# Performance work log

Hardware: AMD Instinct MI355X
Metric: run time of the kernel (lower is better)

The kernel has to match this reference:

```python
import jax, jax.numpy as jnp
import numpy as np

N, IN_DIM, OUT_DIM, HEADS = 8192, 256, 64, 2

def setup_inputs() -> dict:
    key = jax.random.key(0)
    k1, k2, k3, k4, k5 = jax.random.split(key, 5)
    x = jax.random.normal(k1, (N, IN_DIM), dtype=jnp.float32)
    adj = jax.random.randint(k2, (N, N), 0, 2, dtype=jnp.int32)
    # nn.Linear(in_dim, out_dim*heads, bias=False): weight [out_dim*heads, in_dim]
    W = jax.random.normal(k3, (OUT_DIM * HEADS, IN_DIM), dtype=jnp.float32) / np.sqrt(IN_DIM)
    attn_l = jax.random.normal(k4, (HEADS, OUT_DIM), dtype=jnp.float32)
    attn_r = jax.random.normal(k5, (HEADS, OUT_DIM), dtype=jnp.float32)
    return {"x": x, "adj": adj, "W": W, "attn_l": attn_l, "attn_r": attn_r}

def reference(x, adj, W, attn_l, attn_r):
    n = x.shape[0]
    h = (x @ W.T).reshape(n, HEADS, OUT_DIM)          # [N, H, D]
    el = jnp.einsum('nhd,hd->nh', h, attn_l)           # [N, H]
    er = jnp.einsum('nhd,hd->nh', h, attn_r)           # [N, H]
    e = el[:, None, :] + er[None, :, :]                # [N, N, H]
    e = jnp.where(adj[:, :, None] == 0, -jnp.inf, e)
    a = jax.nn.softmax(e, axis=1)                      # softmax over source nodes j
    out = jnp.einsum('ijh,jhd->ihd', a, h)             # [N, H, D]
    return out.reshape(n, HEADS * OUT_DIM)
```

## Files before the change

kernel.cpp:

```cpp
#include <hip/hip_runtime.h>
#include <cstdint>
#include <cstddef>

#define N_NODES 8192
#define IN_DIM  256
#define OUT_DIM 64
#define HEADS   2
#define FEAT    128
#define NTILES  9
#define ACC_STRIDE 132
#define KSPLIT  8

typedef __bf16 bf16x8 __attribute__((ext_vector_type(8)));
typedef float  f32x4  __attribute__((ext_vector_type(4)));
typedef int    i32x4  __attribute__((ext_vector_type(4)));
typedef unsigned uu32x4 __attribute__((ext_vector_type(4)));

static __device__ __forceinline__ unsigned short f2bf(float f) {
  unsigned u = __float_as_uint(f);
  u += 0x7FFFu + ((u >> 16) & 1u);
  return (unsigned short)(u >> 16);
}

__global__ __launch_bounds__(256) void k_prep(const float* __restrict__ x,
                                              const float* __restrict__ W,
                                              const float* __restrict__ attn_r,
                                              uint4* __restrict__ frag) {
  const int kb = blockIdx.x;
  const int tid = threadIdx.x;
  const int tx = tid & 15, ty = tid >> 4;
  const int j0 = kb * 32;

  __shared__ float xs[32][68];
  __shared__ float wl[128][68];
  __shared__ unsigned short pk[32][146];

  float acc[2][8] = {};

  for (int kc = 0; kc < IN_DIM; kc += 64) {
    __syncthreads();
#pragma unroll
    for (int p = 0; p < 2; p++) {
      const int slot = p*256 + tid;
      const int r = slot >> 4, k4 = slot & 15;
      *(float4*)&xs[r][k4*4] = *(const float4*)(x + (size_t)(j0 + r)*IN_DIM + kc + k4*4);
    }
#pragma unroll
    for (int p = 0; p < 8; p++) {
      const int slot = p*256 + tid;
      const int r = slot >> 4, k4 = slot & 15;
      *(float4*)&wl[r][k4*4] = *(const float4*)(W + (size_t)r*IN_DIM + kc + k4*4);
    }
    __syncthreads();
#pragma unroll
    for (int k4 = 0; k4 < 16; k4++) {
      float4 xr[2], wr[8];
#pragma unroll
      for (int i = 0; i < 2; i++) xr[i] = *(const float4*)&xs[ty + i*16][k4*4];
#pragma unroll
      for (int jj = 0; jj < 8; jj++) wr[jj] = *(const float4*)&wl[tx + jj*16][k4*4];
#pragma unroll
      for (int i = 0; i < 2; i++)
#pragma unroll
        for (int jj = 0; jj < 8; jj++)
          acc[i][jj] += xr[i].x*wr[jj].x + xr[i].y*wr[jj].y +
                        xr[i].z*wr[jj].z + xr[i].w*wr[jj].w;
    }
  }

  float ar[8];
#pragma unroll
  for (int jj = 0; jj < 8; jj++)
    ar[jj] = attn_r[((jj >> 2)) * OUT_DIM + ((tx + jj*16) & 63)];
  float e0[2] = {}, e1[2] = {};
#pragma unroll
  for (int i = 0; i < 2; i++) {
#pragma unroll
    for (int jj = 0; jj < 4; jj++) e0[i] += acc[i][jj] * ar[jj];
#pragma unroll
    for (int jj = 4; jj < 8; jj++) e1[i] += acc[i][jj] * ar[jj];
  }
#pragma unroll
  for (int m = 1; m <= 8; m <<= 1) {
#pragma unroll
    for (int i = 0; i < 2; i++) {
      e0[i] += __shfl_xor(e0[i], m);
      e1[i] += __shfl_xor(e1[i], m);
    }
  }
  float w0[2], w1[2];
#pragma unroll
  for (int i = 0; i < 2; i++) { w0[i] = __expf(e0[i]); w1[i] = __expf(e1[i]); }

#pragma unroll
  for (int i = 0; i < 2; i++) {
    const int row = ty + i*16;
#pragma unroll
    for (int jj = 0; jj < 8; jj++)
      pk[row][tx + jj*16] = f2bf((jj < 4 ? w0[i] : w1[i]) * acc[i][jj]);
    pk[row][128 + tx] = (tx == 0) ? f2bf(w0[i]) : (tx == 1) ? f2bf(w1[i]) : 0;
  }
  __syncthreads();

#pragma unroll
  for (int t = 0; t < 3; t++) {
    const int wid = t*256 + tid;
    if (wid < 576) {
      const int l = wid & 63, n = wid >> 6;
      const int col = n*16 + (l & 15), jb = (l >> 4) * 8;
      uint4 o;
      o.x = (unsigned)pk[jb+0][col] | ((unsigned)pk[jb+1][col] << 16);
      o.y = (unsigned)pk[jb+2][col] | ((unsigned)pk[jb+3][col] << 16);
      o.z = (unsigned)pk[jb+4][col] | ((unsigned)pk[jb+5][col] << 16);
      o.w = (unsigned)pk[jb+6][col] | ((unsigned)pk[jb+7][col] << 16);
      frag[((size_t)kb*NTILES + n)*64 + l] = o;
    }
  }
}

__global__ __launch_bounds__(256, 2) void k_main(const int* __restrict__ adj,
                                                 const uint4* __restrict__ fragB,
                                                 float* __restrict__ accum) {
  const int mb = blockIdx.x >> 3;
  const int ks = blockIdx.x & 7;
  const int tid = threadIdx.x;
  const int wave = tid >> 6, lane = tid & 63;
  const int m16 = lane & 15, quad = lane >> 4;

  __shared__ int tile[2][4096];

  const int lr = lane >> 3;
  const int lc = ((lane & 7) ^ lr) << 2;
  const int kb0 = ks * 1024;
  const int* gbase = adj + (size_t)(mb*128)*N_NODES + kb0 + (size_t)lr*N_NODES + lc;

  auto stage = [&](int buf, int kk) {
#pragma unroll
    for (int i = 0; i < 4; ++i) {
      const int c = wave*4 + i;
      const int* g = gbase + (size_t)(c*8)*N_NODES + kk*32;
      __builtin_amdgcn_global_load_lds(
        (const __attribute__((address_space(1))) void*)g,
        (__attribute__((address_space(3))) void*)&tile[buf][c*256],
        16, 0, 0);
    }
  };

  const int r0 = wave*32 + m16;
  const int swz = (r0 & 7) << 4;
  const int a0off = r0*128 + ((quad*32) ^ swz);
  const uu32x4* bb = (const uu32x4*)fragB + lane;

  f32x4 acc0[NTILES], acc1[NTILES];
#pragma unroll
  for (int n = 0; n < NTILES; n++) {
    acc0[n] = (f32x4){0.f, 0.f, 0.f, 0.f};
    acc1[n] = (f32x4){0.f, 0.f, 0.f, 0.f};
  }

  auto conv8 = [&](i32x4 lo, i32x4 hi) -> bf16x8 {
    unsigned u0 = (lo[0] ? 0x3F80u : 0u) | (lo[1] ? 0x3F800000u : 0u);
    unsigned u1 = (lo[2] ? 0x3F80u : 0u) | (lo[3] ? 0x3F800000u : 0u);
    unsigned u2 = (hi[0] ? 0x3F80u : 0u) | (hi[1] ? 0x3F800000u : 0u);
    unsigned u3 = (hi[2] ? 0x3F80u : 0u) | (hi[3] ? 0x3F800000u : 0u);
    uu32x4 u = {u0, u1, u2, u3};
    return __builtin_bit_cast(bf16x8, u);
  };

  stage(0, 0);
  __syncthreads();

  for (int kk = 0; kk < 32; ++kk) {
    const int cur = kk & 1;
    if (kk + 1 < 32) stage(cur ^ 1, kk + 1);

    uu32x4 bv[NTILES];
    {
      const uu32x4* bp = bb + (size_t)(ks*32 + kk)*NTILES*64;
#pragma unroll
      for (int t = 0; t < NTILES; t++) bv[t] = bp[t*64];
    }

    const char* tb = (const char*)&tile[cur][0];
    i32x4 x00 = *(const i32x4*)(tb + a0off);
    i32x4 x01 = *(const i32x4*)(tb + (a0off ^ 16));
    i32x4 x10 = *(const i32x4*)(tb + a0off + 2048);
    i32x4 x11 = *(const i32x4*)(tb + (a0off ^ 16) + 2048);

    bf16x8 af0 = conv8(x00, x01);
    bf16x8 af1 = conv8(x10, x11);
#pragma unroll
    for (int n = 0; n < NTILES; n++) {
      bf16x8 bfr = __builtin_bit_cast(bf16x8, bv[n]);
      acc0[n] = __builtin_amdgcn_mfma_f32_16x16x32_bf16(af0, bfr, acc0[n], 0, 0, 0);
    }
#pragma unroll
    for (int n = 0; n < NTILES; n++) {
      bf16x8 bfr = __builtin_bit_cast(bf16x8, bv[n]);
      acc1[n] = __builtin_amdgcn_mfma_f32_16x16x32_bf16(af1, bfr, acc1[n], 0, 0, 0);
    }

    __syncthreads();
  }

  const int rb0 = mb*128 + wave*32 + quad*4;
  float* op = accum + (size_t)ks*N_NODES*ACC_STRIDE;
#pragma unroll
  for (int n = 0; n < NTILES; n++) {
    if (n == 8 && m16 >= HEADS) continue;
#pragma unroll
    for (int r = 0; r < 4; r++) {
      op[(size_t)(rb0 + r)*ACC_STRIDE + n*16 + m16]      = acc0[n][r];
      op[(size_t)(rb0 + 16 + r)*ACC_STRIDE + n*16 + m16] = acc1[n][r];
    }
  }
}

__global__ void k_div(const float* __restrict__ acc, float* __restrict__ out) {
  const int i = blockIdx.x, c = threadIdx.x;
  const int h = c >> 6;
  float num = 0.f, den = 0.f;
#pragma unroll
  for (int s = 0; s < KSPLIT; s++) {
    const float* p = acc + ((size_t)s*N_NODES + i)*ACC_STRIDE;
    num += p[c];
    den += p[FEAT + h];
  }
  out[(size_t)i*FEAT + c] = num / den;
}

extern "C" void kernel_launch(void* const* d_in, const int* in_sizes, int n_in,
                              void* d_out, int out_size, void* d_ws, size_t ws_size,
                              hipStream_t stream) {
  const float* x      = (const float*)d_in[0];
  const int*   adj    = (const int*)  d_in[1];
  const float* W      = (const float*)d_in[2];
  const float* attn_r = (const float*)d_in[4];

  char* ws = (char*)d_ws;
  uint4* frag = (uint4*)(ws + 0);
  float* acc  = (float*)(ws + 4194304);
  float* out  = (float*)d_out;

  hipLaunchKernelGGL(k_prep, dim3(256),  dim3(256), 0, stream, x, W, attn_r, frag);
  hipLaunchKernelGGL(k_main, dim3(512),  dim3(256), 0, stream, adj, frag, acc);
  hipLaunchKernelGGL(k_div,  dim3(8192), dim3(128), 0, stream, acc, out);
}
```

Baseline: 431.0 us.

## Deepen adjacency prefetch to four LDS buffers and register double-buffer B fragments

The main kernel now uses four LDS tile buffers with a prefetch distance of two, and loads the B fragments for the next step into alternating register sets. A raw s_waitcnt vmcnt(13) plus s_barrier replaces __syncthreads, so outstanding global loads can stay in flight across iterations instead of draining every step. The divide kernel is also vectorised to float4 with 8 rows per block. The changes double LDS use (64KB per block), which may hurt the two-blocks-per-CU occupancy target. The hand-set vmcnt also depends on exact load counts, which makes it fragile.

```diff
diff --git a/kernel.cpp b/kernel.cpp
--- a/kernel.cpp
+++ b/kernel.cpp
@@ -127,12 +127,11 @@
   const int wave = tid >> 6, lane = tid & 63;
   const int m16 = lane & 15, quad = lane >> 4;
 
-  __shared__ int tile[2][4096];
+  __shared__ int tile[4][4096];
 
   const int lr = lane >> 3;
   const int lc = ((lane & 7) ^ lr) << 2;
-  const int kb0 = ks * 1024;
-  const int* gbase = adj + (size_t)(mb*128)*N_NODES + kb0 + (size_t)lr*N_NODES + lc;
+  const int* gbase = adj + (size_t)(mb*128)*N_NODES + ks*1024 + (size_t)lr*N_NODES + lc;
 
   auto stage = [&](int buf, int kk) {
 #pragma unroll
@@ -149,7 +148,7 @@
   const int r0 = wave*32 + m16;
   const int swz = (r0 & 7) << 4;
   const int a0off = r0*128 + ((quad*32) ^ swz);
-  const uu32x4* bb = (const uu32x4*)fragB + lane;
+  const uu32x4* bb = (const uu32x4*)fragB + (size_t)(ks*32)*NTILES*64 + lane;
 
   f32x4 acc0[NTILES], acc1[NTILES];
 #pragma unroll
@@ -158,6 +157,13 @@
     acc1[n] = (f32x4){0.f, 0.f, 0.f, 0.f};
   }
 
+  uu32x4 bvA[NTILES], bvB[NTILES];
+
+  auto loadB = [&](int kk, uu32x4* bv) {
+#pragma unroll
+    for (int t = 0; t < NTILES; t++)
+      bv[t] = bb[(size_t)kk*NTILES*64 + (size_t)t*64];
+  };
   auto conv8 = [&](i32x4 lo, i32x4 hi) -> bf16x8 {
     unsigned u0 = (lo[0] ? 0x3F80u : 0u) | (lo[1] ? 0x3F800000u : 0u);
     unsigned u1 = (lo[2] ? 0x3F80u : 0u) | (lo[3] ? 0x3F800000u : 0u);
@@ -166,27 +172,12 @@
     uu32x4 u = {u0, u1, u2, u3};
     return __builtin_bit_cast(bf16x8, u);
   };
-
-  stage(0, 0);
-  __syncthreads();
-
-  for (int kk = 0; kk < 32; ++kk) {
-    const int cur = kk & 1;
-    if (kk + 1 < 32) stage(cur ^ 1, kk + 1);
-
-    uu32x4 bv[NTILES];
-    {
-      const uu32x4* bp = bb + (size_t)(ks*32 + kk)*NTILES*64;
-#pragma unroll
-      for (int t = 0; t < NTILES; t++) bv[t] = bp[t*64];
-    }
-
-    const char* tb = (const char*)&tile[cur][0];
+  auto substep = [&](int buf, const uu32x4* bv) {
+    const char* tb = (const char*)&tile[0][0] + buf*16384;
     i32x4 x00 = *(const i32x4*)(tb + a0off);
     i32x4 x01 = *(const i32x4*)(tb + (a0off ^ 16));
     i32x4 x10 = *(const i32x4*)(tb + a0off + 2048);
     i32x4 x11 = *(const i32x4*)(tb + (a0off ^ 16) + 2048);
-
     bf16x8 af0 = conv8(x00, x01);
     bf16x8 af1 = conv8(x10, x11);
 #pragma unroll
@@ -199,8 +190,24 @@
       bf16x8 bfr = __builtin_bit_cast(bf16x8, bv[n]);
       acc1[n] = __builtin_amdgcn_mfma_f32_16x16x32_bf16(af1, bfr, acc1[n], 0, 0, 0);
     }
-
-    __syncthreads();
+  };
+
+  stage(0, 0);
+  stage(1, 1);
+  loadB(0, bvA);
+  asm volatile("s_waitcnt vmcnt(13)" ::: "memory");
+  __builtin_amdgcn_s_barrier();
+
+  for (int k = 0; k < 32; k += 4) {
+#pragma unroll
+    for (int j = 0; j < 4; ++j) {
+      const int kk = k + j;
+      if (kk + 2 < 32) stage((kk + 2) & 3, kk + 2);
+      if (kk + 1 < 32) loadB(kk + 1, (j & 1) ? bvA : bvB);
+      substep(kk & 3, (j & 1) ? bvB : bvA);
+      asm volatile("s_waitcnt vmcnt(13)" ::: "memory");
+      __builtin_amdgcn_s_barrier();
+    }
   }
 
   const int rb0 = mb*128 + wave*32 + quad*4;
@@ -217,16 +224,20 @@
 }
 
 __global__ void k_div(const float* __restrict__ acc, float* __restrict__ out) {
-  const int i = blockIdx.x, c = threadIdx.x;
-  const int h = c >> 6;
-  float num = 0.f, den = 0.f;
+  const int tid = threadIdx.x;
+  const int r = tid >> 5, c4 = (tid & 31) << 2;
+  const int i = blockIdx.x * 8 + r;
+  const int h = c4 >> 6;
+  f32x4 num = (f32x4){0.f, 0.f, 0.f, 0.f};
+  float den = 0.f;
 #pragma unroll
   for (int s = 0; s < KSPLIT; s++) {
     const float* p = acc + ((size_t)s*N_NODES + i)*ACC_STRIDE;
-    num += p[c];
+    num += *(const f32x4*)(p + c4);
     den += p[FEAT + h];
   }
-  out[(size_t)i*FEAT + c] = num / den;
+  f32x4 o = num / (f32x4){den, den, den, den};
+  *(f32x4*)(out + (size_t)i*FEAT + c4) = o;
 }
 
 extern "C" void kernel_launch(void* const* d_in, const int* in_sizes, int n_in,
@@ -244,5 +255,5 @@
 
   hipLaunchKernelGGL(k_prep, dim3(256),  dim3(256), 0, stream, x, W, attn_r, frag);
   hipLaunchKernelGGL(k_main, dim3(512),  dim3(256), 0, stream, adj, frag, acc);
-  hipLaunchKernelGGL(k_div,  dim3(8192), dim3(128), 0, stream, acc, out);
-}
+  hipLaunchKernelGGL(k_div,  dim3(1024), dim3(256), 0, stream, acc, out);
+}
```

New measurement: 429.1 us. No clear change (-0.4%).
